# Optimization experiments

Measured on AMD Instinct MI355X. Metric: run time of the kernel, lower is better.

## Reference

```python
import jax, jax.numpy as jnp
import numpy as np

NU, NM, NT = 200000, 50000, 20000   # users, movies, tags
F, H, L = 64, 128, 2                # genre feat dim, hidden, layers
E1, E2 = 800000, 400000             # rates edges, has_tag edges


def setup_inputs() -> dict:
    key = jax.random.key(0)
    ks = jax.random.split(key, 12)
    s = 1.0 / np.sqrt(H)
    return {
        "genre": jax.random.normal(ks[0], (NM, F), jnp.float32),
        "user_emb": jax.random.normal(ks[1], (NU, H), jnp.float32),
        "tag_emb": jax.random.normal(ks[2], (NT, H), jnp.float32),
        "movie_W": jax.random.normal(ks[3], (H, F), jnp.float32) * (1.0 / np.sqrt(F)),
        "movie_b": jnp.zeros((H,), jnp.float32),
        # per-layer, per-edge-type SAGEConv weights; etype order: [rates, rev_rates, has_tag, tag_of]
        "Wn": jax.random.normal(ks[4], (L, 4, H, H), jnp.float32) * s,  # fc_neigh (no bias)
        "Ws": jax.random.normal(ks[5], (L, 4, H, H), jnp.float32) * s,  # fc_self
        "bs": jnp.zeros((L, 4, H), jnp.float32),                        # fc_self bias
        "rates_u": jax.random.randint(ks[6], (E1,), 0, NU, jnp.int32),
        "rates_m": jax.random.randint(ks[7], (E1,), 0, NM, jnp.int32),
        "tag_m": jax.random.randint(ks[8], (E2,), 0, NM, jnp.int32),
        "tag_t": jax.random.randint(ks[9], (E2,), 0, NT, jnp.int32),
    }


def _sage(h_src, h_dst, src, dst, n_dst, Wn, Wself, b):
    # DGL SAGEConv('mean'): fc_self(h_dst) + fc_neigh(mean_{src->dst} h_src)
    m = h_src[src]                                                        # [E, H] gather
    ssum = jax.ops.segment_sum(m, dst, num_segments=n_dst)                # [n_dst, H]
    cnt = jax.ops.segment_sum(jnp.ones((src.shape[0], 1), h_src.dtype), dst, num_segments=n_dst)
    mean = ssum / jnp.maximum(cnt, 1.0)                                   # zero-degree -> 0
    return h_dst @ Wself.T + b + mean @ Wn.T


def reference(genre, user_emb, tag_emb, movie_W, movie_b, Wn, Ws, bs,
              rates_u, rates_m, tag_m, tag_t):
    hu = user_emb
    hm = genre @ movie_W.T + movie_b
    ht = tag_emb
    for l in range(L):
        # HeteroGraphConv(aggregate='sum'): movie receives 'rates' + 'tag_of'
        new_m = (_sage(hu, hm, rates_u, rates_m, NM, Wn[l, 0], Ws[l, 0], bs[l, 0])
                 + _sage(ht, hm, tag_t, tag_m, NM, Wn[l, 3], Ws[l, 3], bs[l, 3]))
        new_u = _sage(hm, hu, rates_m, rates_u, NU, Wn[l, 1], Ws[l, 1], bs[l, 1])  # rev_rates
        new_t = _sage(hm, ht, tag_m, tag_t, NT, Wn[l, 2], Ws[l, 2], bs[l, 2])      # has_tag
        # dropout in eval mode (identity), then LeakyReLU(0.1)
        hu = jax.nn.leaky_relu(new_u, 0.1)
        hm = jax.nn.leaky_relu(new_m, 0.1)
        ht = jax.nn.leaky_relu(new_t, 0.1)
    return hu, hm
```

## Files before the change

kernel.cpp:

```cpp
#include <hip/hip_runtime.h>
#include <stdint.h>


#define NUSR 200000
#define NMOV 50000
#define NTAG 20000
#define FDIM 64
#define HDIM 128
#define NE1  800000
#define NE2  400000

#define OFF_RM 0
#define OFF_RU (NMOV)
#define OFF_TM (NMOV + NUSR)
#define OFF_TT (NMOV + NUSR + NMOV)
#define NTOT   (2 * NMOV + NUSR + NTAG)
#define ETOT   (2 * NE1 + 2 * NE2)
#define WHH    (HDIM * HDIM)

#define WTOT (8192 + 2 * 7 * WHH)
#define BREP 768

#define NB0 196
#define NB1 196
#define NB2 98
#define NB3 157
#define NB  (NB0 + NB1 + NB2 + NB3)
#define S1_EPB 8192
#define S1_B0 98
#define S1_B1 98
#define S1_B2 49
#define S1_B3 49
#define S1_NBLK (S1_B0 + S1_B1 + S1_B2 + S1_B3)
#define CAP 6144

typedef short bf16x8 __attribute__((ext_vector_type(8)));
typedef float f32x4 __attribute__((ext_vector_type(4)));

static inline int cdiv(int a, int b) { return (a + b - 1) / b; }

__device__ __forceinline__ float bf2f(unsigned short u) {
    union { unsigned int i; float f; } c;
    c.i = ((unsigned int)u) << 16;
    return c.f;
}
__device__ __forceinline__ unsigned short f2bf(float f) {
    union { float f; unsigned int i; } c;
    c.f = f;
    unsigned int i = c.i;
    return (unsigned short)((i + 0x7fffu + ((i >> 16) & 1u)) >> 16);
}

__device__ __forceinline__ void gload_lds16(const unsigned short* g, unsigned short* l) {
    __builtin_amdgcn_global_load_lds(
        (const __attribute__((address_space(1))) unsigned int*)(g),
        (__attribute__((address_space(3))) unsigned int*)(l), 16, 0, 0);
}

struct SegInfo {
    int e0, eN, sh, sbb, nb;
    const int* dstA;
    const int* srcA;
};
__device__ __forceinline__ SegInfo seg_decode(int blk, const int* ru, const int* rm,
                                              const int* tm, const int* tt) {
    SegInfo s;
    if (blk < S1_B0) {
        s.e0 = blk * S1_EPB; s.eN = NE1; s.sh = 8;  s.sbb = 0;                 s.nb = NB0;
        s.dstA = rm; s.srcA = ru;
    } else if (blk < S1_B0 + S1_B1) {
        s.e0 = (blk - S1_B0) * S1_EPB; s.eN = NE1; s.sh = 10; s.sbb = NB0;     s.nb = NB1;
        s.dstA = ru; s.srcA = rm;
    } else if (blk < S1_B0 + S1_B1 + S1_B2) {
        s.e0 = (blk - S1_B0 - S1_B1) * S1_EPB; s.eN = NE2; s.sh = 9;
        s.sbb = NB0 + NB1; s.nb = NB2;
        s.dstA = tm; s.srcA = tt;
    } else {
        s.e0 = (blk - S1_B0 - S1_B1 - S1_B2) * S1_EPB; s.eN = NE2; s.sh = 7;
        s.sbb = NB0 + NB1 + NB2; s.nb = NB3;
        s.dstA = tt; s.srcA = tm;
    }
    return s;
}

__global__ __launch_bounds__(256) void csr_bin(const int* __restrict__ ru,
                                               const int* __restrict__ rm,
                                               const int* __restrict__ tm,
                                               const int* __restrict__ tt,
                                               int* __restrict__ bcur,
                                               int* __restrict__ tmp) {
    __shared__ int h[256], st[256], gb[256], cu[256];
    __shared__ int rec[S1_EPB];
    __shared__ unsigned short bk[S1_EPB];
    const int t = threadIdx.x;
    h[t] = 0;
    __syncthreads();
    const SegInfo s = seg_decode(blockIdx.x, ru, rm, tm, tt);
    const int mask = (1 << s.sh) - 1;
#pragma unroll 4
    for (int i = 0; i < S1_EPB / 256; ++i) {
        const int e = s.e0 + t + i * 256;
        if (e < s.eN) atomicAdd(&h[s.dstA[e] >> s.sh], 1);
    }
    __syncthreads();
    const int v = h[t];
    cu[t] = v;
    __syncthreads();
    for (int off = 1; off < 256; off <<= 1) {
        const int add = (t >= off) ? cu[t - off] : 0;
        __syncthreads();
        cu[t] += add;
        __syncthreads();
    }
    st[t] = cu[t] - v;
    gb[t] = (t < s.nb && v) ? atomicAdd(&bcur[s.sbb + t], v) : 0;
    cu[t] = st[t];
    __syncthreads();
#pragma unroll 4
    for (int i = 0; i < S1_EPB / 256; ++i) {
        const int e = s.e0 + t + i * 256;
        if (e < s.eN) {
            const int d = s.dstA[e];
            const int lb = d >> s.sh;
            const int r = ((d & mask) << 18) | s.srcA[e];
            const int p = atomicAdd(&cu[lb], 1);
            rec[p] = r;
            bk[p] = (unsigned short)lb;
        }
    }
    __syncthreads();
    const int ecount = min(S1_EPB, s.eN - s.e0);
    for (int q = t; q < ecount; q += 256) {
        const int lb = bk[q];
        tmp[gb[lb] + (q - st[lb])] = rec[q];
    }
}

__global__ __launch_bounds__(256) void csr_sort(const int* __restrict__ tmp,
                                                const int* __restrict__ bbase,
                                                int* __restrict__ rowptr,
                                                int* __restrict__ sorted) {
    __shared__ int h[1024];
    __shared__ int part[256];
    __shared__ int outb[CAP];
    const int b = blockIdx.x;
    const int t = threadIdx.x;
    int c0, nctr;
    if (b < NB0)                 { c0 = OFF_RM + (b << 8);                nctr = min(256,  NMOV - (b << 8)); }
    else if (b < NB0 + NB1)      { const int j = b - NB0;                 c0 = OFF_RU + (j << 10); nctr = min(1024, NUSR - (j << 10)); }
    else if (b < NB0 + NB1 + NB2){ const int j = b - NB0 - NB1;           c0 = OFF_TM + (j << 9);  nctr = min(512,  NMOV - (j << 9)); }
    else                         { const int j = b - NB0 - NB1 - NB2;     c0 = OFF_TT + (j << 7);  nctr = min(128,  NTAG - (j << 7)); }
    for (int k = t; k < 1024; k += 256) h[k] = 0;
    __syncthreads();
    const int lo = bbase[b], hi = bbase[b + 1];
    const int n = hi - lo;
    for (int e = lo + t; e < hi; e += 256) atomicAdd(&h[tmp[e] >> 18], 1);
    __syncthreads();
    const int b4 = t * 4;
    const int a0 = h[b4], a1 = h[b4 + 1], a2 = h[b4 + 2], a3 = h[b4 + 3];
    const int sum = a0 + a1 + a2 + a3;
    part[t] = sum;
    __syncthreads();
    for (int off = 1; off < 256; off <<= 1) {
        const int add = (t >= off) ? part[t - off] : 0;
        __syncthreads();
        part[t] += add;
        __syncthreads();
    }
    int run = part[t] - sum;
    h[b4] = run; run += a0;
    h[b4 + 1] = run; run += a1;
    h[b4 + 2] = run; run += a2;
    h[b4 + 3] = run;
    __syncthreads();
    for (int k = t; k < nctr; k += 256) rowptr[c0 + k] = lo + h[k];
    __syncthreads();
    if (n <= CAP) {
        for (int e = lo + t; e < hi; e += 256) {
            const int r = tmp[e];
            const int p = atomicAdd(&h[r >> 18], 1);
            outb[p] = r & 0x3FFFF;
        }
        __syncthreads();
        for (int q = t; q < n; q += 256) sorted[lo + q] = outb[q];
    } else {
        for (int e = lo + t; e < hi; e += 256) {
            const int r = tmp[e];
            const int p = atomicAdd(&h[r >> 18], 1);
            sorted[lo + p] = r & 0x3FFFF;
        }
    }
}

__global__ __launch_bounds__(256) void prep_all(
    const float* __restrict__ i0, unsigned short* __restrict__ o0, int n0,
    const float* __restrict__ i1, unsigned short* __restrict__ o1, int n1,
    const float* __restrict__ i2, unsigned short* __restrict__ o2, int n2,
    int gcvt,
    const float* __restrict__ movie_W, const float* __restrict__ movie_b,
    const float* __restrict__ Wn, const float* __restrict__ Ws,
    const float* __restrict__ bs,
    unsigned short* __restrict__ WB, float* __restrict__ BB,
    int* __restrict__ bcnt) {
    if ((int)blockIdx.x < gcvt) {
        int i = blockIdx.x * 256 + threadIdx.x;
        const float* in; unsigned short* out;
        if (i < n0) { in = i0; out = o0; }
        else if (i < n0 + n1) { in = i1; out = o1; i -= n0; }
        else if (i < n0 + n1 + n2) { in = i2; out = o2; i -= n0 + n1; }
        else return;
        const float4 v = ((const float4*)in)[i];
        ushort4 o;
        o.x = f2bf(v.x); o.y = f2bf(v.y); o.z = f2bf(v.z); o.w = f2bf(v.w);
        ((ushort4*)out)[i] = o;
        return;
    }
    const int i = (blockIdx.x - gcvt) * 256 + threadIdx.x;
    if (i <= NB) bcnt[i] = 0;
    if (i < BREP) {
        const int seg = i >> 7, c = i & 127;
        float bv;
        if (seg == 0)      bv = movie_b[c];
        else if (seg == 1) bv = bs[0 * 512 + 1 * 128 + c];
        else if (seg == 2) bv = bs[0 * 512 + 2 * 128 + c];
        else if (seg == 3) bv = bs[0 * 512 + 0 * 128 + c] + bs[0 * 512 + 3 * 128 + c];
        else if (seg == 4) bv = bs[1 * 512 + 1 * 128 + c];
        else               bv = bs[1 * 512 + 0 * 128 + c] + bs[1 * 512 + 3 * 128 + c];
#pragma unroll
        for (int r = 0; r < 8; ++r) BB[r * BREP + i] = bv;
    }
    if (i < WTOT) {
        float v;
        int dest;
        if (i < 8192) {
            v = movie_W[i];
            const int r0 = i >> 6, c0 = i & 63;
            dest = (r0 << 6) + ((((c0 >> 3) ^ (r0 & 7)) << 3) | (c0 & 7));
        } else {
            const int j = i - 8192;
            const int l = j / (7 * WHH);
            const int rr = j % (7 * WHH);
            const int e = rr / WHH;
            const int o = rr % WHH;
            if (e < 4) v = Wn[(l * 4 + e) * WHH + o];
            else if (e == 4) v = Ws[(l * 4 + 1) * WHH + o];
            else if (e == 5) v = Ws[(l * 4 + 2) * WHH + o];
            else v = Ws[(l * 4 + 0) * WHH + o] + Ws[(l * 4 + 3) * WHH + o];
            const int r0 = o >> 7, c0 = o & 127;
            dest = 8192 + l * 7 * WHH + e * WHH +
                   (r0 << 7) + ((((c0 >> 3) ^ (r0 & 7)) << 3) | (c0 & 7));
        }
        const unsigned short bf = f2bf(v);
#pragma unroll
        for (int r = 0; r < 8; ++r) WB[(size_t)r * WTOT + dest] = bf;
    }
}

__global__ __launch_bounds__(256) void agg4(
    const unsigned short* __restrict__ f0, const int* __restrict__ rp0, unsigned short* __restrict__ o0,
    const unsigned short* __restrict__ f1, const int* __restrict__ rp1, unsigned short* __restrict__ o1,
    const unsigned short* __restrict__ f2, const int* __restrict__ rp2, unsigned short* __restrict__ o2,
    const unsigned short* __restrict__ f3, const int* __restrict__ rp3, unsigned short* __restrict__ o3,
    int c0, int c1, int c2, int c3,
    const int* __restrict__ sorted) {
    int g = blockIdx.x * 16 + (threadIdx.x >> 4);
    const unsigned short* feat; const int* rp; unsigned short* out;
    if (g < c0) { feat = f0; rp = rp0; out = o0; }
    else if (g < c1) { feat = f1; rp = rp1; out = o1; g -= c0; }
    else if (g < c2) { feat = f2; rp = rp2; out = o2; g -= c1; }
    else if (g < c3) { feat = f3; rp = rp3; out = o3; g -= c2; }
    else return;
    const int lane = threadIdx.x & 15;
    const int s = rp[g], e = rp[g + 1];
    float a[8];
#pragma unroll
    for (int k = 0; k < 8; ++k) a[k] = 0.f;
    int j = s;
    for (; j + 1 < e; j += 2) {
        const int s0 = sorted[j], s1 = sorted[j + 1];
        const bf16x8 v0 = *(const bf16x8*)&feat[(size_t)s0 * HDIM + lane * 8];
        const bf16x8 v1 = *(const bf16x8*)&feat[(size_t)s1 * HDIM + lane * 8];
#pragma unroll
        for (int k = 0; k < 8; ++k) a[k] += bf2f((unsigned short)v0[k]) + bf2f((unsigned short)v1[k]);
    }
    if (j < e) {
        const int s0 = sorted[j];
        const bf16x8 v0 = *(const bf16x8*)&feat[(size_t)s0 * HDIM + lane * 8];
#pragma unroll
        for (int k = 0; k < 8; ++k) a[k] += bf2f((unsigned short)v0[k]);
    }
    const float sc = (e > s) ? 1.0f / (float)(e - s) : 0.0f;
    bf16x8 o;
#pragma unroll
    for (int k = 0; k < 8; ++k) o[k] = (short)f2bf(a[k] * sc);
    *(bf16x8*)&out[(size_t)g * HDIM + lane * 8] = o;
}

template <int K, bool TWO, bool HAS_ADD, bool HAS_BIAS, bool LEAKY, bool OUT_F32>
__device__ __forceinline__ void tile_core_lds(
    unsigned short* wlds,
    const unsigned short* __restrict__ X1, const unsigned short* __restrict__ W1s,
    const unsigned short* __restrict__ X2, const unsigned short* __restrict__ W2s,
    const unsigned short* __restrict__ addv, const float* __restrict__ bias,
    void* __restrict__ out, int n, int blk) {
    constexpr int NC = K / 32;
    constexpr int PASSES = (128 * K) / 2048;
    const int t = threadIdx.x;
    const int lane = t & 63;
    const int wv = t >> 6;
    const int fr = lane & 15, fq = lane >> 4;
    const int swz = fr & 7;
    const int r = blk * 64 + wv * 16 + fr;
    const int rc = (r < n) ? r : (n - 1);

#pragma unroll
    for (int p = 0; p < PASSES; ++p)
        gload_lds16(W1s + (p * 256 + t) * 8, wlds + (p * 256 + t) * 8);

    bf16x8 xf[NC];
    {
        const unsigned short* xp = X1 + (size_t)rc * K + fq * 8;
#pragma unroll
        for (int c = 0; c < NC; ++c) xf[c] = *(const bf16x8*)(xp + c * 32);
    }

    f32x4 acc[8];
#pragma unroll
    for (int nn = 0; nn < 8; ++nn) acc[nn] = (f32x4){0.f, 0.f, 0.f, 0.f};

    __syncthreads();

#pragma unroll
    for (int nn = 0; nn < 8; ++nn) {
        const int rowoff = (nn * 16 + fr) * K;
#pragma unroll
        for (int c = 0; c < NC; ++c) {
            const bf16x8 wf = *(const bf16x8*)&wlds[rowoff + (((fq + 4 * c) ^ swz) << 3)];
            acc[nn] = __builtin_amdgcn_mfma_f32_16x16x32_bf16(wf, xf[c], acc[nn], 0, 0, 0);
        }
    }

    if (TWO) {
        __syncthreads();
#pragma unroll
        for (int p = 0; p < PASSES; ++p)
            gload_lds16(W2s + (p * 256 + t) * 8, wlds + (p * 256 + t) * 8);
        {
            const unsigned short* xp = X2 + (size_t)rc * K + fq * 8;
#pragma unroll
            for (int c = 0; c < NC; ++c) xf[c] = *(const bf16x8*)(xp + c * 32);
        }
        __syncthreads();
#pragma unroll
        for (int nn = 0; nn < 8; ++nn) {
            const int rowoff = (nn * 16 + fr) * K;
#pragma unroll
            for (int c = 0; c < NC; ++c) {
                const bf16x8 wf = *(const bf16x8*)&wlds[rowoff + (((fq + 4 * c) ^ swz) << 3)];
                acc[nn] = __builtin_amdgcn_mfma_f32_16x16x32_bf16(wf, xf[c], acc[nn], 0, 0, 0);
            }
        }
    }

    if (r < n) {
#pragma unroll
        for (int nn = 0; nn < 8; ++nn) {
            const int c0 = nn * 16 + fq * 4;
            float v0 = acc[nn][0], v1 = acc[nn][1], v2 = acc[nn][2], v3 = acc[nn][3];
            if (HAS_BIAS) {
                const float4 bv = *(const float4*)&bias[c0];
                v0 += bv.x; v1 += bv.y; v2 += bv.z; v3 += bv.w;
            }
            if (HAS_ADD) {
                const ushort4 ad = *(const ushort4*)&addv[(size_t)r * HDIM + c0];
                v0 += bf2f(ad.x); v1 += bf2f(ad.y); v2 += bf2f(ad.z); v3 += bf2f(ad.w);
            }
            if (LEAKY) {
                v0 = v0 > 0.f ? v0 : 0.1f * v0;
                v1 = v1 > 0.f ? v1 : 0.1f * v1;
                v2 = v2 > 0.f ? v2 : 0.1f * v2;
                v3 = v3 > 0.f ? v3 : 0.1f * v3;
            }
            if (OUT_F32) {
                float4 o; o.x = v0; o.y = v1; o.z = v2; o.w = v3;
                *(float4*)&((float*)out)[(size_t)r * HDIM + c0] = o;
            } else {
                ushort4 o;
                o.x = f2bf(v0); o.y = f2bf(v1); o.z = f2bf(v2); o.w = f2bf(v3);
                *(ushort4*)&((unsigned short*)out)[(size_t)r * HDIM + c0] = o;
            }
        }
    }
}

__global__ __launch_bounds__(256, 5) void hist_genre(
    const int* __restrict__ ru, const int* __restrict__ rm,
    const int* __restrict__ tm, const int* __restrict__ tt,
    int* __restrict__ bcnt, int nhist,
    const unsigned short* __restrict__ X, const unsigned short* __restrict__ WB,
    const float* __restrict__ BB, unsigned short* __restrict__ out, int n) {
    __shared__ __align__(16) unsigned short wlds[128 * FDIM];
    const int b = blockIdx.x;
    if (b < nhist) {
        int* h = (int*)wlds;
        const int t = threadIdx.x;
        h[t] = 0;
        __syncthreads();
        const SegInfo s = seg_decode(b, ru, rm, tm, tt);
#pragma unroll 4
        for (int i = 0; i < S1_EPB / 256; ++i) {
            const int e = s.e0 + t + i * 256;
            if (e < s.eN) atomicAdd(&h[s.dstA[e] >> s.sh], 1);
        }
        __syncthreads();
        if (t < s.nb) {
            const int c = h[t];
            if (c) atomicAdd(&bcnt[s.sbb + t], c);
        }
        return;
    }
    const int gb = b - nhist;
    const int rep = gb & 7;
    tile_core_lds<FDIM, false, false, true, false, false>(
        wlds, X, WB + (size_t)rep * WTOT, nullptr, nullptr, nullptr,
        BB + rep * BREP, out, n, gb);
}

__global__ __launch_bounds__(256, 5) void bscan_pre2(
    const int* __restrict__ bcnt, int* __restrict__ bbase, int* __restrict__ bcur,
    int* __restrict__ rowptr,
    const unsigned short* __restrict__ Xa, unsigned short* __restrict__ oa, int na, int nba,
    const unsigned short* __restrict__ Xb, unsigned short* __restrict__ ob, int nb_,
    const unsigned short* __restrict__ WB, int offA, int offB) {
    __shared__ __align__(16) unsigned short wlds[128 * HDIM];
    const int b = blockIdx.x;
    if (b == 0) {
        int* sh = (int*)wlds;
        const int t = threadIdx.x;
        int v[3];
        int s = 0;
#pragma unroll
        for (int k = 0; k < 3; ++k) {
            const int idx = t * 3 + k;
            v[k] = (idx < NB) ? bcnt[idx] : 0;
            s += v[k];
        }
        sh[t] = s;
        __syncthreads();
        for (int off = 1; off < 256; off <<= 1) {
            const int add = (t >= off) ? sh[t - off] : 0;
            __syncthreads();
            sh[t] += add;
            __syncthreads();
        }
        int run = sh[t] - s;
#pragma unroll
        for (int k = 0; k < 3; ++k) {
            const int idx = t * 3 + k;
            if (idx < NB) { bbase[idx] = run; bcur[idx] = run; }
            run += v[k];
        }
        if (t == 255) bbase[NB] = run;
        if (t == 0) rowptr[NTOT] = ETOT;
        return;
    }
    const int pb = b - 1;
    const int rep = pb & 7;
    const unsigned short* WR = WB + (size_t)rep * WTOT;
    if (pb < nba)
        tile_core_lds<HDIM, false, false, false, false, false>(
            wlds, Xa, WR + offA, nullptr, nullptr, nullptr, nullptr, oa, na, pb);
    else
        tile_core_lds<HDIM, false, false, false, false, false>(
            wlds, Xb, WR + offB, nullptr, nullptr, nullptr, nullptr, ob, nb_, pb - nba);
}

__global__ __launch_bounds__(256, 5) void gemm_pre2(
    const unsigned short* __restrict__ Xa, unsigned short* __restrict__ oa, int na, int nba,
    const unsigned short* __restrict__ Xb, unsigned short* __restrict__ ob, int nb_,
    const unsigned short* __restrict__ WB, int offA, int offB) {
    __shared__ __align__(16) unsigned short wlds[128 * HDIM];
    const int b = blockIdx.x;
    const int rep = b & 7;
    const unsigned short* WR = WB + (size_t)rep * WTOT;
    if (b < nba)
        tile_core_lds<HDIM, false, false, false, false, false>(
            wlds, Xa, WR + offA, nullptr, nullptr, nullptr, nullptr, oa, na, b);
    else
        tile_core_lds<HDIM, false, false, false, false, false>(
            wlds, Xb, WR + offB, nullptr, nullptr, nullptr, nullptr, ob, nb_, b - nba);
}

__global__ __launch_bounds__(256, 5) void upd_l0(
    const unsigned short* __restrict__ ub, const unsigned short* __restrict__ U1v,
    unsigned short* __restrict__ U1o,
    const unsigned short* __restrict__ hm0, const unsigned short* __restrict__ M1,
    const unsigned short* __restrict__ M2v, unsigned short* __restrict__ M2o,
    const unsigned short* __restrict__ tb, const unsigned short* __restrict__ T2v,
    unsigned short* __restrict__ T3o,
    const unsigned short* __restrict__ WB, const float* __restrict__ BB,
    int gu, int gm, int gt) {
    __shared__ __align__(16) unsigned short wlds[128 * HDIM];
    const int b = blockIdx.x;
    const int rep = b & 7;
    const unsigned short* WL0 = WB + (size_t)rep * WTOT + 8192;
    const float* BR = BB + rep * BREP;
    if (b < gu) {
        tile_core_lds<HDIM, false, true, true, true, false>(
            wlds, ub, WL0 + 4 * WHH, nullptr, nullptr, U1v, BR + 128, U1o, NUSR, b);
    } else if (b < gu + gm) {
        tile_core_lds<HDIM, true, true, true, true, false>(
            wlds, hm0, WL0 + 6 * WHH, M1, WL0 + 0 * WHH, M2v, BR + 384, M2o, NMOV, b - gu);
    } else {
        tile_core_lds<HDIM, true, false, true, true, false>(
            wlds, tb, WL0 + 5 * WHH, T2v, WL0 + 2 * WHH, nullptr, BR + 256, T3o, NTAG, b - gu - gm);
    }
}

__global__ __launch_bounds__(256, 5) void upd_l1(
    const unsigned short* __restrict__ U1, const unsigned short* __restrict__ U2v,
    float* __restrict__ out_u,
    const unsigned short* __restrict__ M2, const unsigned short* __restrict__ M1,
    const unsigned short* __restrict__ M3v, float* __restrict__ out_m,
    const unsigned short* __restrict__ WB, const float* __restrict__ BB,
    int gu, int gm) {
    __shared__ __align__(16) unsigned short wlds[128 * HDIM];
    const int b = blockIdx.x;
    const int rep = b & 7;
    const unsigned short* WL1 = WB + (size_t)rep * WTOT + 8192 + 7 * WHH;
    const float* BR = BB + rep * BREP;
    if (b < gu) {
        tile_core_lds<HDIM, false, true, true, true, true>(
            wlds, U1, WL1 + 4 * WHH, nullptr, nullptr, U2v, BR + 512, out_u, NUSR, b);
    } else {
        tile_core_lds<HDIM, true, true, true, true, true>(
            wlds, M2, WL1 + 6 * WHH, M1, WL1 + 0 * WHH, M3v, BR + 640, out_m, NMOV, b - gu);
    }
}

extern "C" void kernel_launch(void* const* d_in, const int* in_sizes, int n_in,
                              void* d_out, int out_size, void* d_ws, size_t ws_size,
                              hipStream_t stream) {
    const float* genre    = (const float*)d_in[0];
    const float* user_emb = (const float*)d_in[1];
    const float* tag_emb  = (const float*)d_in[2];
    const float* movie_W  = (const float*)d_in[3];
    const float* movie_b  = (const float*)d_in[4];
    const float* Wn       = (const float*)d_in[5];
    const float* Wsf      = (const float*)d_in[6];
    const float* bsf      = (const float*)d_in[7];
    const int* rates_u    = (const int*)d_in[8];
    const int* rates_m    = (const int*)d_in[9];
    const int* tag_m      = (const int*)d_in[10];
    const int* tag_t      = (const int*)d_in[11];

    float* out_u = (float*)d_out;
    float* out_m = out_u + (size_t)NUSR * HDIM;

    char* w = (char*)d_ws;
    auto alloc = [&](size_t bytes) -> char* {
        char* p = w;
        w += (bytes + 511) & ~(size_t)511;
        return p;
    };
    unsigned short* ub  = (unsigned short*)alloc((size_t)NUSR * HDIM * 2);
    unsigned short* tb  = (unsigned short*)alloc((size_t)NTAG * HDIM * 2);
    unsigned short* gb  = (unsigned short*)alloc((size_t)NMOV * FDIM * 2);
    unsigned short* hm0 = (unsigned short*)alloc((size_t)NMOV * HDIM * 2);
    unsigned short* U1  = (unsigned short*)alloc((size_t)NUSR * HDIM * 2);
    unsigned short* M1  = (unsigned short*)alloc((size_t)NMOV * HDIM * 2);
    unsigned short* M2  = (unsigned short*)alloc((size_t)NMOV * HDIM * 2);
    unsigned short* M3  = (unsigned short*)alloc((size_t)NMOV * HDIM * 2);
    unsigned short* T1  = (unsigned short*)alloc((size_t)NTAG * HDIM * 2);
    unsigned short* T2  = (unsigned short*)alloc((size_t)NTAG * HDIM * 2);
    unsigned short* T3  = (unsigned short*)alloc((size_t)NTAG * HDIM * 2);
    unsigned short* WB  = (unsigned short*)alloc((size_t)8 * WTOT * 2);
    float* BB           = (float*)alloc((size_t)8 * BREP * 4);
    int* rowptr         = (int*)alloc((size_t)(NTOT + 1) * 4);
    int* sorted         = (int*)alloc((size_t)ETOT * 4);
    int* tmpb           = (int*)alloc((size_t)ETOT * 4);
    int* bcnt           = (int*)alloc((size_t)(NB + 1) * 4);
    int* bbase          = (int*)alloc((size_t)(NB + 1) * 4);
    int* bcur           = (int*)alloc((size_t)(NB + 1) * 4);

    const int GU = cdiv(NUSR, 64), GM = cdiv(NMOV, 64), GT = cdiv(NTAG, 64);

    const int n0 = NUSR * HDIM / 4, n1 = NTAG * HDIM / 4, n2 = NMOV * FDIM / 4;
    const int GCVT = cdiv(n0 + n1 + n2, 256);
    const int GWT  = cdiv(WTOT, 256);
    prep_all<<<GCVT + GWT, 256, 0, stream>>>(user_emb, ub, n0, tag_emb, tb, n1, genre, gb, n2,
                                             GCVT, movie_W, movie_b, Wn, Wsf, bsf, WB, BB, bcnt);

    hist_genre<<<S1_NBLK + GM, 256, 0, stream>>>(rates_u, rates_m, tag_m, tag_t, bcnt, S1_NBLK,
                                                 gb, WB, BB, hm0, NMOV);

    bscan_pre2<<<1 + GM + GT, 256, 0, stream>>>(bcnt, bbase, bcur, rowptr,
                                                hm0, M3, NMOV, GM, tb, T1, NTAG,
                                                WB, 8192 + 1 * WHH, 8192 + 3 * WHH);

    csr_bin<<<S1_NBLK, 256, 0, stream>>>(rates_u, rates_m, tag_m, tag_t, bcur, tmpb);
    csr_sort<<<NB, 256, 0, stream>>>(tmpb, bbase, rowptr, sorted);

    agg4<<<cdiv(NTOT, 16), 256, 0, stream>>>(
        M3, rowptr + OFF_RU, U1,
        ub, rowptr + OFF_RM, M1,
        T1, rowptr + OFF_TM, M2,
        hm0, rowptr + OFF_TT, T2,
        NUSR, NUSR + NMOV, NUSR + 2 * NMOV, NTOT, sorted);
    upd_l0<<<GU + GM + GT, 256, 0, stream>>>(ub, U1, U1, hm0, M1, M2, M2,
                                             tb, T2, T3, WB, BB, GU, GM, GT);

    gemm_pre2<<<GM + GT, 256, 0, stream>>>(M2, M3, NMOV, GM, T3, T1, NTAG,
                                           WB, 8192 + 7 * WHH + 1 * WHH, 8192 + 7 * WHH + 3 * WHH);
    agg4<<<cdiv(NUSR + 2 * NMOV, 16), 256, 0, stream>>>(
        M3, rowptr + OFF_RU, ub,
        U1, rowptr + OFF_RM, M1,
        T1, rowptr + OFF_TM, hm0,
        nullptr, nullptr, nullptr,
        NUSR, NUSR + NMOV, NUSR + 2 * NMOV, NUSR + 2 * NMOV, sorted);
    upd_l1<<<GU + GM, 256, 0, stream>>>(U1, ub, out_u, M2, M1, hm0, out_m,
                                        WB, BB, GU, GM);
}
```

Baseline: 390.1 us.

## Fuse user-side mean aggregation into the user update GEMM kernel

```diff
diff --git a/kernel.cpp b/kernel.cpp
--- a/kernel.cpp
+++ b/kernel.cpp
@@ -393,6 +393,118 @@
     }
 }
 
+template <bool OUT_F32>
+__global__ __launch_bounds__(256, 3) void fused_user(
+    const unsigned short* __restrict__ X,
+    const unsigned short* __restrict__ GT,
+    const int* __restrict__ rp, const int* __restrict__ sorted,
+    const unsigned short* __restrict__ WB, int woff,
+    const float* __restrict__ BB, int boff,
+    void* __restrict__ out, int n) {
+    __shared__ __align__(16) unsigned short wlds[128 * HDIM];
+    __shared__ __align__(16) unsigned short alds[64 * HDIM];
+    const int t = threadIdx.x;
+    const int lane = t & 63;
+    const int wv = t >> 6;
+    const int fr = lane & 15, fq = lane >> 4;
+    const int swz = fr & 7;
+    const int rep = blockIdx.x & 7;
+    const unsigned short* Ws = WB + (size_t)rep * WTOT + woff;
+    const float* bias = BB + rep * BREP + boff;
+    const int r = blockIdx.x * 64 + wv * 16 + fr;
+    const int rc = (r < n) ? r : (n - 1);
+
+#pragma unroll
+    for (int p = 0; p < 8; ++p)
+        gload_lds16(Ws + (p * 256 + t) * 8, wlds + (p * 256 + t) * 8);
+
+    {
+        const int grp = t >> 4;
+        const int l16 = t & 15;
+#pragma unroll 1
+        for (int rr = 0; rr < 4; ++rr) {
+            const int row_loc = grp * 4 + rr;
+            int grow = blockIdx.x * 64 + row_loc;
+            if (grow >= n) grow = n - 1;
+            const int s = rp[grow], e = rp[grow + 1];
+            float a[8];
+#pragma unroll
+            for (int k = 0; k < 8; ++k) a[k] = 0.f;
+            int j = s;
+            for (; j + 1 < e; j += 2) {
+                const int s0 = sorted[j], s1 = sorted[j + 1];
+                const bf16x8 v0 = *(const bf16x8*)&GT[(size_t)s0 * HDIM + l16 * 8];
+                const bf16x8 v1 = *(const bf16x8*)&GT[(size_t)s1 * HDIM + l16 * 8];
+#pragma unroll
+                for (int k = 0; k < 8; ++k)
+                    a[k] += bf2f((unsigned short)v0[k]) + bf2f((unsigned short)v1[k]);
+            }
+            if (j < e) {
+                const int s0 = sorted[j];
+                const bf16x8 v0 = *(const bf16x8*)&GT[(size_t)s0 * HDIM + l16 * 8];
+#pragma unroll
+                for (int k = 0; k < 8; ++k) a[k] += bf2f((unsigned short)v0[k]);
+            }
+            const float sc = (e > s) ? 1.0f / (float)(e - s) : 0.0f;
+            bf16x8 o;
+#pragma unroll
+            for (int k = 0; k < 8; ++k) o[k] = (short)f2bf(a[k] * sc);
+            *(bf16x8*)&alds[row_loc * HDIM + ((l16 ^ (row_loc & 7)) << 3)] = o;
+        }
+    }
+
+    bf16x8 xf[4];
+    {
+        const unsigned short* xp = X + (size_t)rc * HDIM + fq * 8;
+#pragma unroll
+        for (int c = 0; c < 4; ++c) xf[c] = *(const bf16x8*)(xp + c * 32);
+    }
+
+    f32x4 acc[8];
+#pragma unroll
+    for (int nn = 0; nn < 8; ++nn) acc[nn] = (f32x4){0.f, 0.f, 0.f, 0.f};
+
+    __syncthreads();
+
+#pragma unroll
+    for (int nn = 0; nn < 8; ++nn) {
+        const int rowoff = (nn * 16 + fr) * HDIM;
+#pragma unroll
+        for (int c = 0; c < 4; ++c) {
+            const bf16x8 wf = *(const bf16x8*)&wlds[rowoff + (((fq + 4 * c) ^ swz) << 3)];
+            acc[nn] = __builtin_amdgcn_mfma_f32_16x16x32_bf16(wf, xf[c], acc[nn], 0, 0, 0);
+        }
+    }
+
+    if (r < n) {
+        const int row_loc = wv * 16 + fr;
+#pragma unroll
+        for (int nn = 0; nn < 8; ++nn) {
+            const int c0 = nn * 16 + fq * 4;
+            const int ci = c0 >> 3;
+            const ushort4 ad = *(const ushort4*)&alds[row_loc * HDIM +
+                                                      ((ci ^ (row_loc & 7)) << 3) + (c0 & 7)];
+            const float4 bv = *(const float4*)&bias[c0];
+            float v0 = acc[nn][0] + bv.x + bf2f(ad.x);
+            float v1 = acc[nn][1] + bv.y + bf2f(ad.y);
+            float v2 = acc[nn][2] + bv.z + bf2f(ad.z);
+            float v3 = acc[nn][3] + bv.w + bf2f(ad.w);
+            v0 = v0 > 0.f ? v0 : 0.1f * v0;
+            v1 = v1 > 0.f ? v1 : 0.1f * v1;
+            v2 = v2 > 0.f ? v2 : 0.1f * v2;
+            v3 = v3 > 0.f ? v3 : 0.1f * v3;
+            if (OUT_F32) {
+                float4 o; o.x = v0; o.y = v1; o.z = v2; o.w = v3;
+                *(float4*)&((float*)out)[(size_t)r * HDIM + c0] = o;
+            } else {
+                ushort4 o;
+                o.x = f2bf(v0); o.y = f2bf(v1); o.z = f2bf(v2); o.w = f2bf(v3);
+                *(ushort4*)&((unsigned short*)out)[(size_t)r * HDIM + c0] = o;
+            }
+        }
+    }
+}
+
 __global__ __launch_bounds__(256, 5) void hist_genre(
     const int* __restrict__ ru, const int* __restrict__ rm,
     const int* __restrict__ tm, const int* __restrict__ tt,
@@ -492,50 +604,37 @@
 }
 
 __global__ __launch_bounds__(256, 5) void upd_l0(
-    const unsigned short* __restrict__ ub, const unsigned short* __restrict__ U1v,
-    unsigned short* __restrict__ U1o,
     const unsigned short* __restrict__ hm0, const unsigned short* __restrict__ M1,
     const unsigned short* __restrict__ M2v, unsigned short* __restrict__ M2o,
     const unsigned short* __restrict__ tb, const unsigned short* __restrict__ T2v,
     unsigned short* __restrict__ T3o,
     const unsigned short* __restrict__ WB, const float* __restrict__ BB,
-    int gu, int gm, int gt) {
+    int gm, int gt) {
     __shared__ __align__(16) unsigned short wlds[128 * HDIM];
     const int b = blockIdx.x;
     const int rep = b & 7;
     const unsigned short* WL0 = WB + (size_t)rep * WTOT + 8192;
     const float* BR = BB + rep * BREP;
-    if (b < gu) {
-        tile_core_lds<HDIM, false, true, true, true, false>(
-            wlds, ub, WL0 + 4 * WHH, nullptr, nullptr, U1v, BR + 128, U1o, NUSR, b);
-    } else if (b < gu + gm) {
+    if (b < gm) {
         tile_core_lds<HDIM, true, true, true, true, false>(
-            wlds, hm0, WL0 + 6 * WHH, M1, WL0 + 0 * WHH, M2v, BR + 384, M2o, NMOV, b - gu);
+            wlds, hm0, WL0 + 6 * WHH, M1, WL0 + 0 * WHH, M2v, BR + 384, M2o, NMOV, b);
     } else {
         tile_core_lds<HDIM, true, false, true, true, false>(
-            wlds, tb, WL0 + 5 * WHH, T2v, WL0 + 2 * WHH, nullptr, BR + 256, T3o, NTAG, b - gu - gm);
+            wlds, tb, WL0 + 5 * WHH, T2v, WL0 + 2 * WHH, nullptr, BR + 256, T3o, NTAG, b - gm);
     }
 }
 
 __global__ __launch_bounds__(256, 5) void upd_l1(
-    const unsigned short* __restrict__ U1, const unsigned short* __restrict__ U2v,
-    float* __restrict__ out_u,
     const unsigned short* __restrict__ M2, const unsigned short* __restrict__ M1,
     const unsigned short* __restrict__ M3v, float* __restrict__ out_m,
-    const unsigned short* __restrict__ WB, const float* __restrict__ BB,
-    int gu, int gm) {
+    const unsigned short* __restrict__ WB, const float* __restrict__ BB) {
     __shared__ __align__(16) unsigned short wlds[128 * HDIM];
     const int b = blockIdx.x;
     const int rep = b & 7;
     const unsigned short* WL1 = WB + (size_t)rep * WTOT + 8192 + 7 * WHH;
     const float* BR = BB + rep * BREP;
-    if (b < gu) {
-        tile_core_lds<HDIM, false, true, true, true, true>(
-            wlds, U1, WL1 + 4 * WHH, nullptr, nullptr, U2v, BR + 512, out_u, NUSR, b);
-    } else {
-        tile_core_lds<HDIM, true, true, true, true, true>(
-            wlds, M2, WL1 + 6 * WHH, M1, WL1 + 0 * WHH, M3v, BR + 640, out_m, NMOV, b - gu);
-    }
+    tile_core_lds<HDIM, true, true, true, true, true>(
+        wlds, M2, WL1 + 6 * WHH, M1, WL1 + 0 * WHH, M3v, BR + 640, out_m, NMOV, b);
 }
 
 extern "C" void kernel_launch(void* const* d_in, const int* in_sizes, int n_in,
@@ -601,23 +700,25 @@
     csr_bin<<<S1_NBLK, 256, 0, stream>>>(rates_u, rates_m, tag_m, tag_t, bcur, tmpb);
     csr_sort<<<NB, 256, 0, stream>>>(tmpb, bbase, rowptr, sorted);
 
-    agg4<<<cdiv(NTOT, 16), 256, 0, stream>>>(
-        M3, rowptr + OFF_RU, U1,
+    agg4<<<cdiv(2 * NMOV + NTAG, 16), 256, 0, stream>>>(
         ub, rowptr + OFF_RM, M1,
         T1, rowptr + OFF_TM, M2,
         hm0, rowptr + OFF_TT, T2,
-        NUSR, NUSR + NMOV, NUSR + 2 * NMOV, NTOT, sorted);
-    upd_l0<<<GU + GM + GT, 256, 0, stream>>>(ub, U1, U1, hm0, M1, M2, M2,
-                                             tb, T2, T3, WB, BB, GU, GM, GT);
+        nullptr, nullptr, nullptr,
+        NMOV, 2 * NMOV, 2 * NMOV + NTAG, 2 * NMOV + NTAG, sorted);
+    fused_user<false><<<GU, 256, 0, stream>>>(ub, M3, rowptr + OFF_RU, sorted,
+                                              WB, 8192 + 4 * WHH, BB, 128, U1, NUSR);
+    upd_l0<<<GM + GT, 256, 0, stream>>>(hm0, M1, M2, M2, tb, T2, T3, WB, BB, GM, GT);
 
     gemm_pre2<<<GM + GT, 256, 0, stream>>>(M2, M3, NMOV, GM, T3, T1, NTAG,
                                            WB, 8192 + 7 * WHH + 1 * WHH, 8192 + 7 * WHH + 3 * WHH);
-    agg4<<<cdiv(NUSR + 2 * NMOV, 16), 256, 0, stream>>>(
-        M3, rowptr + OFF_RU, ub,
+    agg4<<<cdiv(2 * NMOV, 16), 256, 0, stream>>>(
         U1, rowptr + OFF_RM, M1,
         T1, rowptr + OFF_TM, hm0,
         nullptr, nullptr, nullptr,
-        NUSR, NUSR + NMOV, NUSR + 2 * NMOV, NUSR + 2 * NMOV, sorted);
-    upd_l1<<<GU + GM, 256, 0, stream>>>(U1, ub, out_u, M2, M1, hm0, out_m,
-                                        WB, BB, GU, GM);
-}
+        nullptr, nullptr, nullptr,
+        NMOV, 2 * NMOV, 2 * NMOV, 2 * NMOV, sorted);
+    fused_user<true><<<GU, 256, 0, stream>>>(U1, M3, rowptr + OFF_RU, sorted,
+                                             WB, 8192 + 7 * WHH + 4 * WHH, BB, 512, out_u, NUSR);
+    upd_l1<<<GM, 256, 0, stream>>>(M2, M1, hm0, out_m, WB, BB);
+}
```

After: 432.2 us. 1.11x slower.
